# Kernel optimization log

Measured on AMD Instinct MI355X. Metric: run time of the kernel, lower is better.

Reference implementation:

```python
import jax, jax.numpy as jnp
import numpy as np
from jax.scipy.special import gammaln, xlogy

DIM = 1536
HEADS = 8
DK = 64
DV = 64
BS = 128
N = 1536
NRPF = 192  # num_rel_pos_features, divisible by 6
B = 2


def _positional_embed(n, feat):
    # [2n-1, feat] relative positional basis (exponential, central-mask, gamma),
    # each duplicated with sign(d) asymmetric variant.
    f = feat // 6
    d = jnp.arange(-n + 1, n, dtype=jnp.float32)
    ad = jnp.abs(d)[:, None]  # [2n-1, 1]
    # exponential: log-spaced half lives
    half_life = 2.0 ** jnp.linspace(3.0, float(np.log2(n)), f)
    e_exp = jnp.exp(-float(np.log(2.0)) / half_life[None, :] * ad)
    # central mask: 1 if |d| < 2^i - 1
    widths = 2.0 ** jnp.arange(1, f + 1, dtype=jnp.float32) - 1.0
    e_cm = (widths[None, :] > ad).astype(jnp.float32)
    # gamma pdf, linearly spaced means
    std = n / (2.0 * f)
    mean = jnp.linspace(n / f, float(n), f)[None, :]
    conc = (mean / std) ** 2
    rate = mean / (std ** 2)
    log_unnorm = xlogy(conc - 1.0, ad) - rate * ad
    log_norm = gammaln(conc) - conc * jnp.log(rate)
    probs = jnp.exp(log_unnorm - log_norm) + 1e-8
    e_g = probs / jnp.max(probs, axis=-1, keepdims=True)
    emb = jnp.concatenate([e_exp, e_cm, e_g], axis=-1)  # [2n-1, 3f]
    return jnp.concatenate([emb, jnp.sign(d)[:, None] * emb], axis=-1)  # [2n-1, 6f]


def _relative_shift(t):
    # [B, H, N, 2N-1] -> [B, H, N, N] (Transformer-XL shift)
    b, h, t1, t2 = t.shape
    t = jnp.concatenate([jnp.zeros_like(t[..., :1]), t], axis=-1)  # [.., t2+1]
    t = t.reshape(b, h, t2 + 1, t1)[:, :, 1:, :].reshape(b, h, t1, t2)
    return t[..., :t1]


def setup_inputs() -> dict:
    key = jax.random.key(0)
    ks = jax.random.split(key, 10)
    x = jax.random.normal(ks[0], (B, N, DIM), dtype=jnp.float32)
    Wq = jax.random.normal(ks[1], (DIM, HEADS * DK), dtype=jnp.float32) * 0.02
    Wk = jax.random.normal(ks[2], (DIM, HEADS * DK), dtype=jnp.float32) * 0.02
    Wv = jax.random.normal(ks[3], (DIM, HEADS * DV), dtype=jnp.float32) * 0.02
    Wrel = jax.random.normal(ks[4], (NRPF, HEADS * DK), dtype=jnp.float32) * 0.02
    rel_content_bias = jax.random.normal(ks[5], (1, HEADS, 1, DK), dtype=jnp.float32)
    rel_pos_bias = jax.random.normal(ks[6], (1, HEADS, 1, DK), dtype=jnp.float32)
    # to_out is zero-init in the original; use small random so the output/grads are non-trivial
    Wo = jax.random.normal(ks[7], (HEADS * DV, DIM), dtype=jnp.float32) * 0.02
    bo = jnp.zeros((DIM,), dtype=jnp.float32)
    pos_embed = _positional_embed(N, NRPF)  # [2N-1, NRPF]
    # BigBird block-local window mask: blocks bi attend to blocks bi-1..bi+1
    bi = np.arange(N) // BS
    local_mask = jnp.asarray(np.abs(bi[:, None] - bi[None, :]) <= 1)  # [N, N] bool
    # a few global tokens per batch
    is_global = jnp.zeros((B, N), dtype=bool).at[:, :4].set(True)
    return {"x": x, "Wq": Wq, "Wk": Wk, "Wv": Wv, "Wrel": Wrel,
            "rel_content_bias": rel_content_bias, "rel_pos_bias": rel_pos_bias,
            "Wo": Wo, "bo": bo, "pos_embed": pos_embed,
            "local_mask": local_mask, "is_global": is_global}


def reference(x, Wq, Wk, Wv, Wrel, rel_content_bias, rel_pos_bias, Wo, bo,
              pos_embed, local_mask, is_global):
    b, n, _ = x.shape
    h, dk = rel_content_bias.shape[1], rel_content_bias.shape[-1]
    dv = Wv.shape[-1] // h
    scale = dk ** -0.5
    q = (x @ Wq).reshape(b, n, h, dk).transpose(0, 2, 1, 3) * scale  # [b,h,n,dk]
    k = (x @ Wk).reshape(b, n, h, dk).transpose(0, 2, 1, 3)
    v = (x @ Wv).reshape(b, n, h, dv).transpose(0, 2, 1, 3)
    content_logits = jnp.einsum('bhid,bhjd->bhij', q + rel_content_bias, k)
    rel_k = (pos_embed @ Wrel).reshape(2 * n - 1, h, dk).transpose(1, 0, 2)  # [h,2n-1,dk]
    rel_logits = jnp.einsum('bhid,hjd->bhij', q + rel_pos_bias, rel_k)  # [b,h,n,2n-1]
    logits = content_logits + _relative_shift(rel_logits)
    attn_bool = (local_mask[None, None] | is_global[:, None, :, None]
                 | is_global[:, None, None, :])
    logits = jnp.where(attn_bool, logits.astype(jnp.float32), -jnp.inf)
    attn = jax.nn.softmax(logits, axis=-1)
    out = jnp.einsum('bhij,bhjd->bhid', attn, v.astype(jnp.float32))
    out = out.astype(x.dtype).transpose(0, 2, 1, 3).reshape(b, n, h * dv)
    return out @ Wo + bo
```

## Files before the change

### kernel.cpp

```cpp
#include <hip/hip_runtime.h>
#include <math.h>

#define NSEQ 1536
#define HD3  1536
#define RKLD 512
#define RLEN 3071
#define NB   12

typedef __attribute__((ext_vector_type(8))) short bf16x8;
typedef __attribute__((ext_vector_type(4))) float f32x4;
typedef _Float16 f16x8 __attribute__((ext_vector_type(8)));
typedef _Float16 f16x4 __attribute__((ext_vector_type(4)));

__device__ __forceinline__ unsigned short f2bf(float f) {
    union { float f; unsigned u; } v; v.f = f;
    unsigned r = v.u + 0x7fffu + ((v.u >> 16) & 1u);
    return (unsigned short)(r >> 16);
}
__device__ __forceinline__ float bf2f(unsigned short s) {
    union { unsigned u; float f; } v; v.u = ((unsigned)s) << 16;
    return v.f;
}
__device__ __forceinline__ void cp16(const void* g, void* l) {
    __builtin_amdgcn_global_load_lds(
        (const __attribute__((address_space(1))) void*)g,
        (__attribute__((address_space(3))) void*)l, 16, 0, 0);
}

#define KSWZ(row, d) ((row) * 64 + (((((d) >> 3) ^ ((row) & 7))) << 3) + ((d) & 7))
#define PSWZ(r, j)   ((r) * 128 + (((((j) >> 3) ^ ((r) & 15))) << 3) + ((j) & 7))
#define VSTR 136

__global__ __launch_bounds__(256) void splitf16(
    const float* __restrict__ X, _Float16* __restrict__ H, int n4)
{
    int i = blockIdx.x * 256 + threadIdx.x;
    if (i >= n4) return;
    float4 v = ((const float4*)X)[i];
    union { _Float16 h[4]; ushort4 u; } c;
    c.h[0] = (_Float16)v.x; c.h[1] = (_Float16)v.y;
    c.h[2] = (_Float16)v.z; c.h[3] = (_Float16)v.w;
    ((ushort4*)H)[i] = c.u;
}

__device__ __forceinline__ void wsplit_body16(
    const float* __restrict__ W, _Float16* __restrict__ T,
    int K, int N, int n_off, int ldt, float scale, int bx, int by)
{
    __shared__ float tile[64][65];
    const int k0 = by * 64, n0 = bx * 64;
    const int t = threadIdx.x;
    const int rr = t >> 4, c4 = (t & 15) * 4;
#pragma unroll
    for (int p = 0; p < 4; ++p) {
        int r = p * 16 + rr;
        float4 v = *(const float4*)(W + (size_t)(k0 + r) * N + n0 + c4);
        tile[r][c4 + 0] = v.x; tile[r][c4 + 1] = v.y;
        tile[r][c4 + 2] = v.z; tile[r][c4 + 3] = v.w;
    }
    __syncthreads();
#pragma unroll
    for (int p = 0; p < 4; ++p) {
        int n = p * 16 + rr;
        union { _Float16 h[4]; ushort4 u; } cc;
        cc.h[0] = (_Float16)(tile[c4 + 0][n] * scale);
        cc.h[1] = (_Float16)(tile[c4 + 1][n] * scale);
        cc.h[2] = (_Float16)(tile[c4 + 2][n] * scale);
        cc.h[3] = (_Float16)(tile[c4 + 3][n] * scale);
        size_t o = (size_t)(n_off + n0 + n) * ldt + k0 + c4;
        *(ushort4*)(T + o) = cc.u;
    }
}

__global__ __launch_bounds__(256) void wsplit_all(
    const float* __restrict__ Wq, const float* __restrict__ Wk,
    const float* __restrict__ Wv, const float* __restrict__ Wo,
    const float* __restrict__ Wrel,
    _Float16* __restrict__ Tqkv, _Float16* __restrict__ To,
    _Float16* __restrict__ Trel)
{
    const int z = blockIdx.z;
    if (z < 3) {
        const float* W = (z == 0) ? Wq : (z == 1) ? Wk : Wv;
        wsplit_body16(W, Tqkv, 1536, 512, z * 512, 1536,
                      (z == 0) ? 0.125f : 1.f, blockIdx.x, blockIdx.y);
    } else if (z == 3) {
        wsplit_body16(Wo, To, 512, 1536, 0, 512, 1.f, blockIdx.y, blockIdx.x);
    } else {
        if (blockIdx.y >= 3) return;
        wsplit_body16(Wrel, Trel, 192, 512, 0, 192, 1.f, blockIdx.x, blockIdx.y);
    }
}

__global__ __launch_bounds__(256) void gemm_f16k(
    const _Float16* __restrict__ A,
    const _Float16* __restrict__ B,
    const float* __restrict__ bias, float* __restrict__ C,
    int M, int N, int K)
{
    __shared__ _Float16 sA[2][4096];
    __shared__ _Float16 sB[2][4096];
    const int t = threadIdx.x;
    const int wave = t >> 6, lane = t & 63;
    const int nwg = gridDim.x * gridDim.y;
    const int lin = blockIdx.y * gridDim.x + blockIdx.x;
    const int swz = (lin & 7) * (nwg >> 3) + (lin >> 3);
    const int bx = swz % gridDim.x, by = swz / gridDim.x;
    const int m0 = by * 64, n0 = bx * 64;
    const int wm = (wave >> 1) * 32, wn = (wave & 1) * 32;
    const int fr = lane & 15, quad = lane >> 4;

    f32x4 acc[2][2];
#pragma unroll
    for (int i = 0; i < 2; ++i)
#pragma unroll
        for (int j = 0; j < 2; ++j)
#pragma unroll
            for (int c = 0; c < 4; ++c) acc[i][j][c] = 0.f;

    const int nsteps = K >> 6;

#define STAGE(k0, buf)                                                        \
    {                                                                         \
        _Pragma("unroll")                                                     \
        for (int it = 0; it < 2; ++it) {                                      \
            int cidx = it * 256 + t;                                          \
            int row = cidx >> 3, slot = cidx & 7;                             \
            int gch = slot ^ (row & 7);                                       \
            size_t goA = (size_t)(m0 + row) * K + (k0) + gch * 8;             \
            size_t goB = (size_t)(n0 + row) * K + (k0) + gch * 8;             \
            cp16(A + goA, &sA[buf][it * 2048 + wave * 512]);                  \
            cp16(B + goB, &sB[buf][it * 2048 + wave * 512]);                  \
        }                                                                     \
    }

    STAGE(0, 0);
    for (int s = 0; s < nsteps; ++s) {
        const int buf = s & 1;
        __syncthreads();
        if (s + 1 < nsteps) STAGE((s + 1) * 64, buf ^ 1);

        f16x8 fa[2][2], fb[2][2];
#pragma unroll
        for (int ti = 0; ti < 2; ++ti)
#pragma unroll
            for (int kc = 0; kc < 2; ++kc) {
                fa[ti][kc] = *(const f16x8*)&sA[buf][KSWZ(wm + ti * 16 + fr,
                                                          kc * 32 + quad * 8)];
                fb[ti][kc] = *(const f16x8*)&sB[buf][KSWZ(wn + ti * 16 + fr,
                                                          kc * 32 + quad * 8)];
            }
#pragma unroll
        for (int ti = 0; ti < 2; ++ti)
#pragma unroll
            for (int tj = 0; tj < 2; ++tj)
#pragma unroll
                for (int kc = 0; kc < 2; ++kc)
                    acc[ti][tj] = __builtin_amdgcn_mfma_f32_16x16x32_f16(
                        fa[ti][kc], fb[tj][kc], acc[ti][tj], 0, 0, 0);
    }
#undef STAGE

#pragma unroll
    for (int ti = 0; ti < 2; ++ti) {
        int rowb = m0 + wm + ti * 16 + quad * 4;
#pragma unroll
        for (int tj = 0; tj < 2; ++tj) {
            int col = n0 + wn + tj * 16 + fr;
            float bb = bias ? bias[col] : 0.f;
#pragma unroll
            for (int j2 = 0; j2 < 4; ++j2)
                C[(size_t)(rowb + j2) * N + col] = acc[ti][tj][j2] + bb;
        }
    }
}

__global__ __launch_bounds__(256) void drk_kernel(
    const float* __restrict__ rkk, const float* __restrict__ cb,
    const float* __restrict__ rb, float* __restrict__ drk)
{
    int idx = blockIdx.x * 256 + threadIdx.x;
    if (idx >= 8 * RLEN) return;
    int jj = idx >> 3, h = idx & 7;
    const float* rrow = rkk + (size_t)jj * RKLD + h * 64;
    float s0 = 0, s1 = 0, s2 = 0, s3 = 0;
#pragma unroll
    for (int d4 = 0; d4 < 16; ++d4) {
        float4 rv = *(const float4*)(rrow + d4 * 4);
        float dx = rb[h * 64 + d4 * 4 + 0] - cb[h * 64 + d4 * 4 + 0];
        float dy = rb[h * 64 + d4 * 4 + 1] - cb[h * 64 + d4 * 4 + 1];
        float dz = rb[h * 64 + d4 * 4 + 2] - cb[h * 64 + d4 * 4 + 2];
        float dw = rb[h * 64 + d4 * 4 + 3] - cb[h * 64 + d4 * 4 + 3];
        s0 = fmaf(dx, rv.x, s0); s1 = fmaf(dy, rv.y, s1);
        s2 = fmaf(dz, rv.z, s2); s3 = fmaf(dw, rv.w, s3);
    }
    drk[h * RLEN + jj] = (s0 + s1) + (s2 + s3);
}

__global__ __launch_bounds__(256) void relb_mfma(
    const float* __restrict__ qkv, const float* __restrict__ rkk,
    const float* __restrict__ rb, _Float16* __restrict__ relbT)
{
    __shared__ _Float16 sR[8192];
    const int ct = blockIdx.x, bi = blockIdx.y, bh = blockIdx.z;
    const int b = bh >> 3, h = bh & 7;
    const int i0 = bi * 128;
    const int c0 = (bi == 0) ? 0 : (bi - 1) * 128;
    const int jjbase = c0 - i0 - 127 + (NSEQ - 1) + ct * 128;
    const int t = threadIdx.x;
    const int wave = t >> 6, lane = t & 63;
    const int fr = lane & 15, quad = lane >> 4;

#pragma unroll
    for (int it = 0; it < 8; ++it) {
        int lin = it * 256 + t;
        int row = lin >> 4, d4 = (lin & 15) * 4;
        const float* rp = rkk + (size_t)(jjbase + row) * RKLD + h * 64 + d4;
        float4 v = *(const float4*)rp;
        union { _Float16 h[4]; ushort4 u; } cc;
        cc.h[0] = (_Float16)v.x; cc.h[1] = (_Float16)v.y;
        cc.h[2] = (_Float16)v.z; cc.h[3] = (_Float16)v.w;
        *(ushort4*)&sR[KSWZ(row, d4)] = cc.u;
    }
    f16x8 qf[2][2];
    {
        const float* Qg = qkv + ((size_t)(b * NSEQ + i0)) * HD3 + h * 64;
#pragma unroll
        for (int ti = 0; ti < 2; ++ti)
#pragma unroll
            for (int kc = 0; kc < 2; ++kc) {
                int m = wave * 32 + ti * 16 + fr;
                int k8 = kc * 32 + quad * 8;
                const float* qp = Qg + (size_t)m * HD3 + k8;
                const float* cp = rb + h * 64 + k8;
                float4 qa = *(const float4*)qp,  qb = *(const float4*)(qp + 4);
                float4 ca = *(const float4*)cp,  c2 = *(const float4*)(cp + 4);
                _Float16 hx[8] = {
                    (_Float16)(qa.x + ca.x), (_Float16)(qa.y + ca.y),
                    (_Float16)(qa.z + ca.z), (_Float16)(qa.w + ca.w),
                    (_Float16)(qb.x + c2.x), (_Float16)(qb.y + c2.y),
                    (_Float16)(qb.z + c2.z), (_Float16)(qb.w + c2.w)};
                qf[ti][kc] = *(f16x8*)hx;
            }
    }
    __syncthreads();

    f32x4 sacc[2][8];
#pragma unroll
    for (int i = 0; i < 2; ++i)
#pragma unroll
        for (int j = 0; j < 8; ++j)
#pragma unroll
            for (int c = 0; c < 4; ++c) sacc[i][j][c] = 0.f;

#pragma unroll
    for (int kc = 0; kc < 2; ++kc) {
        f16x8 bv[8];
#pragma unroll
        for (int tj = 0; tj < 8; ++tj)
            bv[tj] = *(const f16x8*)&sR[KSWZ(tj * 16 + fr, kc * 32 + quad * 8)];
#pragma unroll
        for (int ti = 0; ti < 2; ++ti)
#pragma unroll
            for (int tj = 0; tj < 8; ++tj)
                sacc[ti][tj] = __builtin_amdgcn_mfma_f32_16x16x32_f16(
                    qf[ti][kc], bv[tj], sacc[ti][tj], 0, 0, 0);
    }

    size_t bb_ = ((size_t)bh * NB + bi) * 512;
#pragma unroll
    for (int ti = 0; ti < 2; ++ti) {
        int mr = wave * 32 + ti * 16 + quad * 4;
#pragma unroll
        for (int tj = 0; tj < 8; ++tj) {
            int ccg = ct * 128 + tj * 16 + fr;
#pragma unroll
            for (int reg = 0; reg < 4; ++reg) {
                int r = mr + reg;
                int jl = ccg - 127 + r;
                if (jl >= 0)
                    relbT[(bb_ + jl) * 128 + r] = (_Float16)sacc[ti][tj][reg];
            }
        }
    }
}

__global__ __launch_bounds__(256) void attn_mfma(
    const float* __restrict__ qkv, const _Float16* __restrict__ relbT,
    const float* __restrict__ rkbuf, const float* __restrict__ drk,
    const float* __restrict__ cb, float* __restrict__ O_part,
    float* __restrict__ l_part)
{
    __shared__ unsigned short sKP[16384];
    __shared__ unsigned short sVt[64 * VSTR];
    __shared__ float p_g[128 * 4];
    __shared__ __align__(16) float vg[4 * 64];
    __shared__ float lg[128];
    const int ct = blockIdx.x, bi = blockIdx.y, bh = blockIdx.z;
    const int b = bh >> 3, h = bh & 7;
    const int i0 = bi * 128;
    const int c0 = (bi == 0) ? 0 : (bi - 1) * 128;
    const int c1 = (bi == NB - 1) ? NSEQ : (bi + 2) * 128;
    const int ctile = c0 + ct * 128;
    const int t = threadIdx.x;
    const int wave = t >> 6, lane = t & 63;
    const int fr = lane & 15, quad = lane >> 4;

    float* Op = O_part + (((size_t)ct * 16 + bh) * NSEQ + i0) * 64;
    float* lp = l_part + ((size_t)ct * 16 + bh) * NSEQ + i0;

    if (ctile >= c1) {
        for (int k2 = t; k2 < 8192; k2 += 256) Op[k2] = 0.f;
        if (t < 128) lp[t] = 0.f;
        return;
    }

    const bool do_g = (ct == 0 && bi >= 2);

    {
        const float* Kg = qkv + ((size_t)(b * NSEQ + ctile)) * HD3 + 512 + h * 64;
#pragma unroll
        for (int it = 0; it < 8; ++it) {
            int lin = it * 256 + t;
            int row = lin >> 4, d4 = (lin & 15) * 4;
            float4 v = *(const float4*)(Kg + (size_t)row * HD3 + d4);
            union { _Float16 h[4]; ushort4 u; } cc;
            cc.h[0] = (_Float16)v.x; cc.h[1] = (_Float16)v.y;
            cc.h[2] = (_Float16)v.z; cc.h[3] = (_Float16)v.w;
            *(ushort4*)&sKP[KSWZ(row, d4)] = cc.u;
        }
    }
    {
        const float* Vg = qkv + ((size_t)(b * NSEQ + ctile)) * HD3 + 1024 + h * 64;
#pragma unroll
        for (int it = 0; it < 2; ++it) {
            int lin = it * 256 + t;
            int r4 = (lin >> 4) * 4, d4 = (lin & 15) * 4;
            float4 v0 = *(const float4*)(Vg + (size_t)(r4 + 0) * HD3 + d4);
            float4 v1 = *(const float4*)(Vg + (size_t)(r4 + 1) * HD3 + d4);
            float4 v2 = *(const float4*)(Vg + (size_t)(r4 + 2) * HD3 + d4);
            float4 v3 = *(const float4*)(Vg + (size_t)(r4 + 3) * HD3 + d4);
            const float* p0 = (const float*)&v0;
            const float* p1 = (const float*)&v1;
            const float* p2 = (const float*)&v2;
            const float* p3 = (const float*)&v3;
#pragma unroll
            for (int dd = 0; dd < 4; ++dd) {
                ushort4 hh;
                hh.x = f2bf(p0[dd]); hh.y = f2bf(p1[dd]);
                hh.z = f2bf(p2[dd]); hh.w = f2bf(p3[dd]);
                *(ushort4*)&sVt[(d4 + dd) * VSTR + r4] = hh;
            }
        }
    }
    if (do_g) {
        if (t < 128) {
            const int r = t;
            const int i = i0 + r;
            const int jjb = NSEQ - 1 - i;
            const float* qrow = qkv + (size_t)(b * NSEQ + i) * HD3 + h * 64;
            const float* krow = qkv + (size_t)(b * NSEQ) * HD3 + 512 + h * 64;
            const float* rrow = rkbuf + (size_t)jjb * RKLD + h * 64;
            float s[4] = {0.f, 0.f, 0.f, 0.f};
#pragma unroll
            for (int d4 = 0; d4 < 16; ++d4) {
                float4 qv = *(const float4*)(qrow + d4 * 4);
                float4 cv = *(const float4*)(cb + h * 64 + d4 * 4);
                float q0 = qv.x + cv.x, q1 = qv.y + cv.y;
                float q2 = qv.z + cv.z, q3 = qv.w + cv.w;
#pragma unroll
                for (int j = 0; j < 4; ++j) {
                    float4 kv = *(const float4*)(krow + (size_t)j * HD3 + d4 * 4);
                    float4 rv = *(const float4*)(rrow + (size_t)j * RKLD + d4 * 4);
                    s[j] = fmaf(q0, kv.x + rv.x, s[j]);
                    s[j] = fmaf(q1, kv.y + rv.y, s[j]);
                    s[j] = fmaf(q2, kv.z + rv.z, s[j]);
                    s[j] = fmaf(q3, kv.w + rv.w, s[j]);
                }
            }
            float l = 0.f;
#pragma unroll
            for (int j = 0; j < 4; ++j) {
                float p = __expf(s[j] + drk[h * RLEN + jjb + j]);
                p_g[r * 4 + j] = p;
                l += p;
            }
            lg[r] = l;
        } else {
            int u = (t - 128) * 2;
#pragma unroll
            for (int w = 0; w < 2; ++w) {
                int idx = u + w;
                vg[idx] = qkv[(size_t)(b * NSEQ + (idx >> 6)) * HD3 + 1024
                              + h * 64 + (idx & 63)];
            }
        }
    }
    f16x8 qf[2][2];
    {
        const float* Qg = qkv + ((size_t)(b * NSEQ + i0)) * HD3 + h * 64;
#pragma unroll
        for (int ti = 0; ti < 2; ++ti)
#pragma unroll
            for (int kc = 0; kc < 2; ++kc) {
                int m = wave * 32 + ti * 16 + fr;
                int k8 = kc * 32 + quad * 8;
                const float* qp = Qg + (size_t)m * HD3 + k8;
                const float* cp = cb + h * 64 + k8;
                float4 qa = *(const float4*)qp,  qb = *(const float4*)(qp + 4);
                float4 ca = *(const float4*)cp,  c2 = *(const float4*)(cp + 4);
                _Float16 hx[8] = {
                    (_Float16)(qa.x + ca.x), (_Float16)(qa.y + ca.y),
                    (_Float16)(qa.z + ca.z), (_Float16)(qa.w + ca.w),
                    (_Float16)(qb.x + c2.x), (_Float16)(qb.y + c2.y),
                    (_Float16)(qb.z + c2.z), (_Float16)(qb.w + c2.w)};
                qf[ti][kc] = *(f16x8*)hx;
            }
    }
    __syncthreads();

    f32x4 sacc[2][8];
#pragma unroll
    for (int i = 0; i < 2; ++i)
#pragma unroll
        for (int j = 0; j < 8; ++j)
#pragma unroll
            for (int c = 0; c < 4; ++c) sacc[i][j][c] = 0.f;

#pragma unroll
    for (int kc = 0; kc < 2; ++kc) {
        f16x8 bv[8];
#pragma unroll
        for (int tj = 0; tj < 8; ++tj)
            bv[tj] = *(const f16x8*)&sKP[KSWZ(tj * 16 + fr, kc * 32 + quad * 8)];
#pragma unroll
        for (int ti = 0; ti < 2; ++ti)
#pragma unroll
            for (int tj = 0; tj < 8; ++tj)
                sacc[ti][tj] = __builtin_amdgcn_mfma_f32_16x16x32_f16(
                    qf[ti][kc], bv[tj], sacc[ti][tj], 0, 0, 0);
    }
    __syncthreads();

    const _Float16* relbase = relbT + (((size_t)bh * NB + bi) * 512 + ct * 128) * 128;
    float lsum[2][4] = {{0.f, 0.f, 0.f, 0.f}, {0.f, 0.f, 0.f, 0.f}};
#pragma unroll
    for (int ti = 0; ti < 2; ++ti) {
        int mr = wave * 32 + ti * 16 + quad * 4;
#pragma unroll
        for (int tj = 0; tj < 8; ++tj) {
            int j = tj * 16 + fr;
            f16x4 rl = *(const f16x4*)&relbase[(size_t)j * 128 + mr];
#pragma unroll
            for (int reg = 0; reg < 4; ++reg) {
                int r = mr + reg;
                float p = __expf(sacc[ti][tj][reg] + (float)rl[reg]);
                unsigned short pb = f2bf(p);
                lsum[ti][reg] += bf2f(pb);
                sKP[PSWZ(r, j)] = pb;
            }
        }
    }
#pragma unroll
    for (int m2 = 1; m2 < 16; m2 <<= 1)
#pragma unroll
        for (int ti = 0; ti < 2; ++ti)
#pragma unroll
            for (int reg = 0; reg < 4; ++reg)
                lsum[ti][reg] += __shfl_xor(lsum[ti][reg], m2, 64);
    if (fr == 0) {
#pragma unroll
        for (int ti = 0; ti < 2; ++ti) {
            int mr = wave * 32 + ti * 16 + quad * 4;
#pragma unroll
            for (int reg = 0; reg < 4; ++reg)
                lp[mr + reg] = lsum[ti][reg] + (do_g ? lg[mr + reg] : 0.f);
        }
    }

    f32x4 oacc[4][2];
#pragma unroll
    for (int i = 0; i < 4; ++i)
#pragma unroll
        for (int j = 0; j < 2; ++j)
#pragma unroll
            for (int c = 0; c < 4; ++c) oacc[i][j][c] = 0.f;

#pragma unroll
    for (int kc = 0; kc < 4; ++kc) {
        bf16x8 pbv[2];
#pragma unroll
        for (int rt2 = 0; rt2 < 2; ++rt2) {
            int r = (wave * 2 + rt2) * 16 + fr;
            pbv[rt2] = *(const bf16x8*)&sKP[PSWZ(r, kc * 32 + quad * 8)];
        }
#pragma unroll
        for (int dt = 0; dt < 4; ++dt) {
            bf16x8 av = *(const bf16x8*)&sVt[(dt * 16 + fr) * VSTR + kc * 32 + quad * 8];
#pragma unroll
            for (int rt2 = 0; rt2 < 2; ++rt2)
                oacc[dt][rt2] = __builtin_amdgcn_mfma_f32_16x16x32_bf16(
                    av, pbv[rt2], oacc[dt][rt2], 0, 0, 0);
        }
    }
#pragma unroll
    for (int rt2 = 0; rt2 < 2; ++rt2) {
        int r = (wave * 2 + rt2) * 16 + fr;
        float pg0 = 0.f, pg1 = 0.f, pg2 = 0.f, pg3 = 0.f;
        if (do_g) {
            pg0 = p_g[r * 4 + 0]; pg1 = p_g[r * 4 + 1];
            pg2 = p_g[r * 4 + 2]; pg3 = p_g[r * 4 + 3];
        }
#pragma unroll
        for (int dt = 0; dt < 4; ++dt) {
            int d = dt * 16 + quad * 4;
            float4 ov = make_float4(oacc[dt][rt2][0], oacc[dt][rt2][1],
                                    oacc[dt][rt2][2], oacc[dt][rt2][3]);
            if (do_g) {
                float4 v0 = *(const float4*)&vg[0 * 64 + d];
                float4 v1 = *(const float4*)&vg[1 * 64 + d];
                float4 v2 = *(const float4*)&vg[2 * 64 + d];
                float4 v3 = *(const float4*)&vg[3 * 64 + d];
                ov.x += pg0 * v0.x + pg1 * v1.x + pg2 * v2.x + pg3 * v3.x;
                ov.y += pg0 * v0.y + pg1 * v1.y + pg2 * v2.y + pg3 * v3.y;
                ov.z += pg0 * v0.z + pg1 * v1.z + pg2 * v2.z + pg3 * v3.z;
                ov.w += pg0 * v0.w + pg1 * v1.w + pg2 * v2.w + pg3 * v3.w;
            }
            *(float4*)(Op + (size_t)r * 64 + d) = ov;
        }
    }
}

__global__ __launch_bounds__(256) void grows_part(
    const float* __restrict__ qkv, const float* __restrict__ rkk,
    const float* __restrict__ drk, const float* __restrict__ cb,
    float* __restrict__ g_O, float* __restrict__ g_l)
{
    __shared__ float qc_s[64];
    __shared__ float p_s[128];
    __shared__ float obuf[4][64];
    __shared__ float lred[2];
    const int chunk = blockIdx.x;
    const int bhi = blockIdx.y;
    const int i = bhi & 3, h = (bhi >> 2) & 7, b = bhi >> 5;
    const int t = threadIdx.x;
    const int c0 = chunk * 128;
    if (t < 64)
        qc_s[t] = qkv[(size_t)(b * NSEQ + i) * HD3 + h * 64 + t] + cb[h * 64 + t];
    __syncthreads();
    if (t < 128) {
        int j = c0 + t;
        const float* krow = qkv + (size_t)(b * NSEQ + j) * HD3 + 512 + h * 64;
        int jj = j - i + (NSEQ - 1);
        const float* rrow = rkk + (size_t)jj * RKLD + h * 64;
        float s0 = 0, s1 = 0, s2 = 0, s3 = 0;
#pragma unroll
        for (int d4 = 0; d4 < 16; ++d4) {
            float4 kv = *(const float4*)(krow + d4 * 4);
            float4 rv = *(const float4*)(rrow + d4 * 4);
            float4 qv = *(const float4*)(&qc_s[d4 * 4]);
            s0 = fmaf(qv.x, kv.x + rv.x, s0);
            s1 = fmaf(qv.y, kv.y + rv.y, s1);
            s2 = fmaf(qv.z, kv.z + rv.z, s2);
            s3 = fmaf(qv.w, kv.w + rv.w, s3);
        }
        float p = __expf((s0 + s1) + (s2 + s3) + drk[h * RLEN + jj]);
        p_s[t] = p;
        float ls = p;
#pragma unroll
        for (int off = 32; off > 0; off >>= 1)
            ls += __shfl_down(ls, off, 64);
        if ((t & 63) == 0) lred[t >> 6] = ls;
    }
    __syncthreads();
    {
        const int d = t & 63, g = t >> 6;
        float a0 = 0, a1 = 0;
        const float* vbase = qkv + (size_t)(b * NSEQ + c0 + g * 32) * HD3 + 1024 + h * 64 + d;
#pragma unroll
        for (int j2 = 0; j2 < 32; j2 += 2) {
            a0 = fmaf(p_s[g * 32 + j2],     vbase[(size_t)j2 * HD3],       a0);
            a1 = fmaf(p_s[g * 32 + j2 + 1], vbase[(size_t)(j2 + 1) * HD3], a1);
        }
        obuf[g][d] = a0 + a1;
    }
    __syncthreads();
    if (t < 64) {
        float o = (obuf[0][t] + obuf[1][t]) + (obuf[2][t] + obuf[3][t]);
        g_O[((size_t)chunk * 64 + bhi) * 64 + t] = o;
        if (t == 0) g_l[chunk * 64 + bhi] = lred[0] + lred[1];
    }
}

__global__ __launch_bounds__(256) void norm_merge(
    const float* __restrict__ O_part, const float* __restrict__ l_part,
    const float* __restrict__ g_O, const float* __restrict__ g_l,
    _Float16* __restrict__ aoh)
{
    const int bh = blockIdx.y, b = bh >> 3, h = bh & 7;
    const int i = blockIdx.x * 16 + (threadIdx.x >> 4);
    const int d4 = threadIdx.x & 15;
    float ox = 0, oy = 0, oz = 0, ow = 0, l = 0;
    if (i < 4) {
        const int bhi = bh * 4 + i;
#pragma unroll
        for (int c = 0; c < 12; ++c) {
            const float* gp = g_O + ((size_t)c * 64 + bhi) * 64 + d4 * 4;
            ox += gp[0]; oy += gp[1]; oz += gp[2]; ow += gp[3];
            l += g_l[c * 64 + bhi];
        }
    } else {
#pragma unroll
        for (int s = 0; s < 3; ++s) {
            const float* Opp = O_part + (((size_t)s * 16 + bh) * NSEQ + i) * 64 + d4 * 4;
            float4 p = *(const float4*)Opp;
            ox += p.x; oy += p.y; oz += p.z; ow += p.w;
            l += l_part[((size_t)s * 16 + bh) * NSEQ + i];
        }
    }
    float inv = 1.f / l;
    union { _Float16 h[4]; ushort4 u; } cc;
    cc.h[0] = (_Float16)(ox * inv); cc.h[1] = (_Float16)(oy * inv);
    cc.h[2] = (_Float16)(oz * inv); cc.h[3] = (_Float16)(ow * inv);
    size_t o = ((size_t)(b * NSEQ + i)) * 512 + h * 64 + d4 * 4;
    *(ushort4*)(aoh + o) = cc.u;
}

extern "C" void kernel_launch(void* const* d_in, const int* in_sizes, int n_in,
                              void* d_out, int out_size, void* d_ws, size_t ws_size,
                              hipStream_t stream)
{
    const float* x    = (const float*)d_in[0];
    const float* Wq   = (const float*)d_in[1];
    const float* Wk   = (const float*)d_in[2];
    const float* Wv   = (const float*)d_in[3];
    const float* Wrel = (const float*)d_in[4];
    const float* cb   = (const float*)d_in[5];
    const float* rb   = (const float*)d_in[6];
    const float* Wo   = (const float*)d_in[7];
    const float* bo   = (const float*)d_in[8];
    const float* pe   = (const float*)d_in[9];
    float* out = (float*)d_out;

    float* ws = (float*)d_ws;
    float* qkv   = ws;
    float* rkbuf = ws + 4718592;
    float* drk   = ws + 6291456;
    _Float16* aoh = (_Float16*)(ws + 6316032);
    _Float16* woh = (_Float16*)(ws + 7888896);
    float* R = ws + 8675328;
    _Float16* relbT = (_Float16*)R;
    _Float16* xh  = (_Float16*)R;
    _Float16* wqh = (_Float16*)(R + 4718592);
    float* g_O = R + 6291456;
    float* g_l = R + 6340608;
    float* O_part = ws + 15753216;
    float* l_part = ws + 20471808;
    _Float16* peh   = (_Float16*)(ws + 20545536);
    _Float16* wrelT = (_Float16*)(ws + 20840448);

    dim3 blk(256);
    splitf16<<<4608, blk, 0, stream>>>(x, xh, 1179648);
    splitf16<<<576, blk, 0, stream>>>(pe, peh, 147408);
    wsplit_all<<<dim3(8, 24, 5), blk, 0, stream>>>(Wq, Wk, Wv, Wo, Wrel,
                                                   wqh, woh, wrelT);
    gemm_f16k<<<dim3(24, 48), blk, 0, stream>>>(xh, wqh, nullptr, qkv,
                                                3072, 1536, 1536);
    gemm_f16k<<<dim3(8, 48), blk, 0, stream>>>(peh, wrelT, nullptr, rkbuf,
                                               3072, 512, 192);
    drk_kernel<<<96, blk, 0, stream>>>(rkbuf, cb, rb, drk);
    relb_mfma<<<dim3(4, 12, 16), blk, 0, stream>>>(qkv, rkbuf, rb, relbT);
    attn_mfma<<<dim3(3, 12, 16), blk, 0, stream>>>(qkv, relbT, rkbuf, drk, cb,
                                                   O_part, l_part);
    grows_part<<<dim3(12, 64), blk, 0, stream>>>(qkv, rkbuf, drk, cb, g_O, g_l);
    norm_merge<<<dim3(96, 16), blk, 0, stream>>>(O_part, l_part, g_O, g_l, aoh);
    gemm_f16k<<<dim3(24, 48), blk, 0, stream>>>(aoh, woh, bo, out,
                                                3072, 1536, 512);
}
```

Baseline: 242.8 us.

## Store QKV and rel-K projections in half precision and load tiles asynchronously

The QKV and relative-key GEMMs now write 16-bit outputs (fp16 for Q/K and rel-K, bf16 for V) instead of fp32. Downstream kernels read these directly, so the per-block fp32-to-half conversions go away and K/rel-K tiles can be copied into LDS with direct global-to-LDS loads. The two input conversion kernels are merged into one launch. This halves intermediate memory traffic at the cost of storing q/k/v and rel-K at reduced precision before the bias add and dot products.

```diff
diff --git a/kernel.cpp b/kernel.cpp
--- a/kernel.cpp
+++ b/kernel.cpp
@@ -21,6 +21,9 @@
     union { unsigned u; float f; } v; v.u = ((unsigned)s) << 16;
     return v.f;
 }
+__device__ __forceinline__ unsigned short f2h(float f) {
+    union { _Float16 h; unsigned short u; } c; c.h = (_Float16)f; return c.u;
+}
 __device__ __forceinline__ void cp16(const void* g, void* l) {
     __builtin_amdgcn_global_load_lds(
         (const __attribute__((address_space(1))) void*)g,
@@ -31,16 +34,25 @@
 #define PSWZ(r, j)   ((r) * 128 + (((((j) >> 3) ^ ((r) & 15))) << 3) + ((j) & 7))
 #define VSTR 136
 
-__global__ __launch_bounds__(256) void splitf16(
-    const float* __restrict__ X, _Float16* __restrict__ H, int n4)
-{
-    int i = blockIdx.x * 256 + threadIdx.x;
-    if (i >= n4) return;
-    float4 v = ((const float4*)X)[i];
+__global__ __launch_bounds__(256) void split2_f16(
+    const float* __restrict__ X, _Float16* __restrict__ HX,
+    const float* __restrict__ P, _Float16* __restrict__ HP)
+{
+    const int bid = blockIdx.x;
+    const float* src; _Float16* dst; int i;
+    if (bid < 4608) {
+        i = bid * 256 + threadIdx.x;
+        src = X; dst = HX;
+    } else {
+        i = (bid - 4608) * 256 + threadIdx.x;
+        if (i >= 147408) return;
+        src = P; dst = HP;
+    }
+    float4 v = ((const float4*)src)[i];
     union { _Float16 h[4]; ushort4 u; } c;
     c.h[0] = (_Float16)v.x; c.h[1] = (_Float16)v.y;
     c.h[2] = (_Float16)v.z; c.h[3] = (_Float16)v.w;
-    ((ushort4*)H)[i] = c.u;
+    ((ushort4*)dst)[i] = c.u;
 }
 
 __device__ __forceinline__ void wsplit_body16(
@@ -95,8 +107,8 @@
 __global__ __launch_bounds__(256) void gemm_f16k(
     const _Float16* __restrict__ A,
     const _Float16* __restrict__ B,
-    const float* __restrict__ bias, float* __restrict__ C,
-    int M, int N, int K)
+    const float* __restrict__ bias, void* __restrict__ C,
+    int M, int N, int K, int omode)
 {
     __shared__ _Float16 sA[2][4096];
     __shared__ _Float16 sB[2][4096];
@@ -161,44 +173,63 @@
     }
 #undef STAGE
 
-#pragma unroll
-    for (int ti = 0; ti < 2; ++ti) {
-        int rowb = m0 + wm + ti * 16 + quad * 4;
-#pragma unroll
-        for (int tj = 0; tj < 2; ++tj) {
-            int col = n0 + wn + tj * 16 + fr;
-            float bb = bias ? bias[col] : 0.f;
-#pragma unroll
-            for (int j2 = 0; j2 < 4; ++j2)
-                C[(size_t)(rowb + j2) * N + col] = acc[ti][tj][j2] + bb;
+    if (omode == 0) {
+        float* Cf = (float*)C;
+#pragma unroll
+        for (int ti = 0; ti < 2; ++ti) {
+            int rowb = m0 + wm + ti * 16 + quad * 4;
+#pragma unroll
+            for (int tj = 0; tj < 2; ++tj) {
+                int col = n0 + wn + tj * 16 + fr;
+                float bb = bias ? bias[col] : 0.f;
+#pragma unroll
+                for (int j2 = 0; j2 < 4; ++j2)
+                    Cf[(size_t)(rowb + j2) * N + col] = acc[ti][tj][j2] + bb;
+            }
+        }
+    } else {
+        unsigned short* Cu = (unsigned short*)C;
+        const bool vb = (omode == 1) && (n0 >= 1024);
+#pragma unroll
+        for (int ti = 0; ti < 2; ++ti) {
+            int rowb = m0 + wm + ti * 16 + quad * 4;
+#pragma unroll
+            for (int tj = 0; tj < 2; ++tj) {
+                int col = n0 + wn + tj * 16 + fr;
+#pragma unroll
+                for (int j2 = 0; j2 < 4; ++j2) {
+                    float v = acc[ti][tj][j2];
+                    Cu[(size_t)(rowb + j2) * N + col] = vb ? f2bf(v) : f2h(v);
+                }
+            }
         }
     }
 }
 
 __global__ __launch_bounds__(256) void drk_kernel(
-    const float* __restrict__ rkk, const float* __restrict__ cb,
+    const _Float16* __restrict__ rkh, const float* __restrict__ cb,
     const float* __restrict__ rb, float* __restrict__ drk)
 {
     int idx = blockIdx.x * 256 + threadIdx.x;
     if (idx >= 8 * RLEN) return;
     int jj = idx >> 3, h = idx & 7;
-    const float* rrow = rkk + (size_t)jj * RKLD + h * 64;
+    const _Float16* rrow = rkh + (size_t)jj * RKLD + h * 64;
     float s0 = 0, s1 = 0, s2 = 0, s3 = 0;
 #pragma unroll
     for (int d4 = 0; d4 < 16; ++d4) {
-        float4 rv = *(const float4*)(rrow + d4 * 4);
+        f16x4 rv = *(const f16x4*)(rrow + d4 * 4);
         float dx = rb[h * 64 + d4 * 4 + 0] - cb[h * 64 + d4 * 4 + 0];
         float dy = rb[h * 64 + d4 * 4 + 1] - cb[h * 64 + d4 * 4 + 1];
         float dz = rb[h * 64 + d4 * 4 + 2] - cb[h * 64 + d4 * 4 + 2];
         float dw = rb[h * 64 + d4 * 4 + 3] - cb[h * 64 + d4 * 4 + 3];
-        s0 = fmaf(dx, rv.x, s0); s1 = fmaf(dy, rv.y, s1);
-        s2 = fmaf(dz, rv.z, s2); s3 = fmaf(dw, rv.w, s3);
+        s0 = fmaf(dx, (float)rv[0], s0); s1 = fmaf(dy, (float)rv[1], s1);
+        s2 = fmaf(dz, (float)rv[2], s2); s3 = fmaf(dw, (float)rv[3], s3);
     }
     drk[h * RLEN + jj] = (s0 + s1) + (s2 + s3);
 }
 
 __global__ __launch_bounds__(256) void relb_mfma(
-    const float* __restrict__ qkv, const float* __restrict__ rkk,
+    const _Float16* __restrict__ qkvh, const _Float16* __restrict__ rkh,
     const float* __restrict__ rb, _Float16* __restrict__ relbT)
 {
     __shared__ _Float16 sR[8192];
@@ -211,35 +242,32 @@
     const int wave = t >> 6, lane = t & 63;
     const int fr = lane & 15, quad = lane >> 4;
 
-#pragma unroll
-    for (int it = 0; it < 8; ++it) {
-        int lin = it * 256 + t;
-        int row = lin >> 4, d4 = (lin & 15) * 4;
-        const float* rp = rkk + (size_t)(jjbase + row) * RKLD + h * 64 + d4;
-        float4 v = *(const float4*)rp;
-        union { _Float16 h[4]; ushort4 u; } cc;
-        cc.h[0] = (_Float16)v.x; cc.h[1] = (_Float16)v.y;
-        cc.h[2] = (_Float16)v.z; cc.h[3] = (_Float16)v.w;
-        *(ushort4*)&sR[KSWZ(row, d4)] = cc.u;
+    {
+        const _Float16* Rg = rkh + (size_t)jjbase * RKLD + h * 64;
+#pragma unroll
+        for (int it = 0; it < 4; ++it) {
+            int cidx = it * 256 + t;
+            int row = cidx >> 3, slot = cidx & 7;
+            int gch = slot ^ (row & 7);
+            cp16(Rg + (size_t)row * RKLD + gch * 8,
+                 &sR[it * 2048 + wave * 512]);
+        }
     }
     f16x8 qf[2][2];
     {
-        const float* Qg = qkv + ((size_t)(b * NSEQ + i0)) * HD3 + h * 64;
+        const _Float16* Qg = qkvh + ((size_t)(b * NSEQ + i0)) * HD3 + h * 64;
 #pragma unroll
         for (int ti = 0; ti < 2; ++ti)
 #pragma unroll
             for (int kc = 0; kc < 2; ++kc) {
                 int m = wave * 32 + ti * 16 + fr;
                 int k8 = kc * 32 + quad * 8;
-                const float* qp = Qg + (size_t)m * HD3 + k8;
+                f16x8 qv = *(const f16x8*)(Qg + (size_t)m * HD3 + k8);
                 const float* cp = rb + h * 64 + k8;
-                float4 qa = *(const float4*)qp,  qb = *(const float4*)(qp + 4);
-                float4 ca = *(const float4*)cp,  c2 = *(const float4*)(cp + 4);
-                _Float16 hx[8] = {
-                    (_Float16)(qa.x + ca.x), (_Float16)(qa.y + ca.y),
-                    (_Float16)(qa.z + ca.z), (_Float16)(qa.w + ca.w),
-                    (_Float16)(qb.x + c2.x), (_Float16)(qb.y + c2.y),
-                    (_Float16)(qb.z + c2.z), (_Float16)(qb.w + c2.w)};
+                _Float16 hx[8];
+#pragma unroll
+                for (int u = 0; u < 8; ++u)
+                    hx[u] = (_Float16)((float)qv[u] + cp[u]);
                 qf[ti][kc] = *(f16x8*)hx;
             }
     }
@@ -286,8 +314,8 @@
 }
 
 __global__ __launch_bounds__(256) void attn_mfma(
-    const float* __restrict__ qkv, const _Float16* __restrict__ relbT,
-    const float* __restrict__ rkbuf, const float* __restrict__ drk,
+    const _Float16* __restrict__ qkvh, const _Float16* __restrict__ relbT,
+    const _Float16* __restrict__ rkh, const float* __restrict__ drk,
     const float* __restrict__ cb, float* __restrict__ O_part,
     float* __restrict__ l_part)
 {
@@ -316,39 +344,38 @@
     }
 
     const bool do_g = (ct == 0 && bi >= 2);
+    const unsigned short* Vall = (const unsigned short*)qkvh;
 
     {
-        const float* Kg = qkv + ((size_t)(b * NSEQ + ctile)) * HD3 + 512 + h * 64;
-#pragma unroll
-        for (int it = 0; it < 8; ++it) {
-            int lin = it * 256 + t;
-            int row = lin >> 4, d4 = (lin & 15) * 4;
-            float4 v = *(const float4*)(Kg + (size_t)row * HD3 + d4);
-            union { _Float16 h[4]; ushort4 u; } cc;
-            cc.h[0] = (_Float16)v.x; cc.h[1] = (_Float16)v.y;
-            cc.h[2] = (_Float16)v.z; cc.h[3] = (_Float16)v.w;
-            *(ushort4*)&sKP[KSWZ(row, d4)] = cc.u;
+        const _Float16* Kg = qkvh + ((size_t)(b * NSEQ + ctile)) * HD3 + 512 + h * 64;
+#pragma unroll
+        for (int it = 0; it < 4; ++it) {
+            int cidx = it * 256 + t;
+            int row = cidx >> 3, slot = cidx & 7;
+            int gch = slot ^ (row & 7);
+            cp16(Kg + (size_t)row * HD3 + gch * 8,
+                 (unsigned short*)&sKP[it * 2048 + wave * 512]);
         }
     }
     {
-        const float* Vg = qkv + ((size_t)(b * NSEQ + ctile)) * HD3 + 1024 + h * 64;
+        const unsigned short* Vg = Vall + ((size_t)(b * NSEQ + ctile)) * HD3
+                                   + 1024 + h * 64;
 #pragma unroll
         for (int it = 0; it < 2; ++it) {
             int lin = it * 256 + t;
             int r4 = (lin >> 4) * 4, d4 = (lin & 15) * 4;
-            float4 v0 = *(const float4*)(Vg + (size_t)(r4 + 0) * HD3 + d4);
-            float4 v1 = *(const float4*)(Vg + (size_t)(r4 + 1) * HD3 + d4);
-            float4 v2 = *(const float4*)(Vg + (size_t)(r4 + 2) * HD3 + d4);
-            float4 v3 = *(const float4*)(Vg + (size_t)(r4 + 3) * HD3 + d4);
-            const float* p0 = (const float*)&v0;
-            const float* p1 = (const float*)&v1;
-            const float* p2 = (const float*)&v2;
-            const float* p3 = (const float*)&v3;
+            ushort4 v0 = *(const ushort4*)(Vg + (size_t)(r4 + 0) * HD3 + d4);
+            ushort4 v1 = *(const ushort4*)(Vg + (size_t)(r4 + 1) * HD3 + d4);
+            ushort4 v2 = *(const ushort4*)(Vg + (size_t)(r4 + 2) * HD3 + d4);
+            ushort4 v3 = *(const ushort4*)(Vg + (size_t)(r4 + 3) * HD3 + d4);
+            const unsigned short* p0 = (const unsigned short*)&v0;
+            const unsigned short* p1 = (const unsigned short*)&v1;
+            const unsigned short* p2 = (const unsigned short*)&v2;
+            const unsigned short* p3 = (const unsigned short*)&v3;
 #pragma unroll
             for (int dd = 0; dd < 4; ++dd) {
                 ushort4 hh;
-                hh.x = f2bf(p0[dd]); hh.y = f2bf(p1[dd]);
-                hh.z = f2bf(p2[dd]); hh.w = f2bf(p3[dd]);
+                hh.x = p0[dd]; hh.y = p1[dd]; hh.z = p2[dd]; hh.w = p3[dd];
                 *(ushort4*)&sVt[(d4 + dd) * VSTR + r4] = hh;
             }
         }
@@ -358,24 +385,24 @@
             const int r = t;
             const int i = i0 + r;
             const int jjb = NSEQ - 1 - i;
-            const float* qrow = qkv + (size_t)(b * NSEQ + i) * HD3 + h * 64;
-            const float* krow = qkv + (size_t)(b * NSEQ) * HD3 + 512 + h * 64;
-            const float* rrow = rkbuf + (size_t)jjb * RKLD + h * 64;
+            const _Float16* qrow = qkvh + (size_t)(b * NSEQ + i) * HD3 + h * 64;
+            const _Float16* krow = qkvh + (size_t)(b * NSEQ) * HD3 + 512 + h * 64;
+            const _Float16* rrow = rkh + (size_t)jjb * RKLD + h * 64;
             float s[4] = {0.f, 0.f, 0.f, 0.f};
 #pragma unroll
             for (int d4 = 0; d4 < 16; ++d4) {
-                float4 qv = *(const float4*)(qrow + d4 * 4);
+                f16x4 qv = *(const f16x4*)(qrow + d4 * 4);
                 float4 cv = *(const float4*)(cb + h * 64 + d4 * 4);
-                float q0 = qv.x + cv.x, q1 = qv.y + cv.y;
-                float q2 = qv.z + cv.z, q3 = qv.w + cv.w;
+                float q0 = (float)qv[0] + cv.x, q1 = (float)qv[1] + cv.y;
+                float q2 = (float)qv[2] + cv.z, q3 = (float)qv[3] + cv.w;
 #pragma unroll
                 for (int j = 0; j < 4; ++j) {
-                    float4 kv = *(const float4*)(krow + (size_t)j * HD3 + d4 * 4);
-                    float4 rv = *(const float4*)(rrow + (size_t)j * RKLD + d4 * 4);
-                    s[j] = fmaf(q0, kv.x + rv.x, s[j]);
-                    s[j] = fmaf(q1, kv.y + rv.y, s[j]);
-                    s[j] = fmaf(q2, kv.z + rv.z, s[j]);
-                    s[j] = fmaf(q3, kv.w + rv.w, s[j]);
+                    f16x4 kv = *(const f16x4*)(krow + (size_t)j * HD3 + d4 * 4);
+                    f16x4 rv = *(const f16x4*)(rrow + (size_t)j * RKLD + d4 * 4);
+                    s[j] = fmaf(q0, (float)kv[0] + (float)rv[0], s[j]);
+                    s[j] = fmaf(q1, (float)kv[1] + (float)rv[1], s[j]);
+                    s[j] = fmaf(q2, (float)kv[2] + (float)rv[2], s[j]);
+                    s[j] = fmaf(q3, (float)kv[3] + (float)rv[3], s[j]);
                 }
             }
             float l = 0.f;
@@ -387,33 +414,31 @@
             }
             lg[r] = l;
         } else {
+            const unsigned short* Vg0 = Vall + (size_t)(b * NSEQ) * HD3
+                                        + 1024 + h * 64;
             int u = (t - 128) * 2;
 #pragma unroll
             for (int w = 0; w < 2; ++w) {
                 int idx = u + w;
-                vg[idx] = qkv[(size_t)(b * NSEQ + (idx >> 6)) * HD3 + 1024
-                              + h * 64 + (idx & 63)];
+                vg[idx] = bf2f(Vg0[(size_t)(idx >> 6) * HD3 + (idx & 63)]);
             }
         }
     }
     f16x8 qf[2][2];
     {
-        const float* Qg = qkv + ((size_t)(b * NSEQ + i0)) * HD3 + h * 64;
+        const _Float16* Qg = qkvh + ((size_t)(b * NSEQ + i0)) * HD3 + h * 64;
 #pragma unroll
         for (int ti = 0; ti < 2; ++ti)
 #pragma unroll
             for (int kc = 0; kc < 2; ++kc) {
                 int m = wave * 32 + ti * 16 + fr;
                 int k8 = kc * 32 + quad * 8;
-                const float* qp = Qg + (size_t)m * HD3 + k8;
+                f16x8 qv = *(const f16x8*)(Qg + (size_t)m * HD3 + k8);
                 const float* cp = cb + h * 64 + k8;
-                float4 qa = *(const float4*)qp,  qb = *(const float4*)(qp + 4);
-                float4 ca = *(const float4*)cp,  c2 = *(const float4*)(cp + 4);
-                _Float16 hx[8] = {
-                    (_Float16)(qa.x + ca.x), (_Float16)(qa.y + ca.y),
-                    (_Float16)(qa.z + ca.z), (_Float16)(qa.w + ca.w),
-                    (_Float16)(qb.x + c2.x), (_Float16)(qb.y + c2.y),
-                    (_Float16)(qb.z + c2.z), (_Float16)(qb.w + c2.w)};
+                _Float16 hx[8];
+#pragma unroll
+                for (int u = 0; u < 8; ++u)
+                    hx[u] = (_Float16)((float)qv[u] + cp[u]);
                 qf[ti][kc] = *(f16x8*)hx;
             }
     }
@@ -532,7 +557,7 @@
 }
 
 __global__ __launch_bounds__(256) void grows_part(
-    const float* __restrict__ qkv, const float* __restrict__ rkk,
+    const _Float16* __restrict__ qkvh, const _Float16* __restrict__ rkh,
     const float* __restrict__ drk, const float* __restrict__ cb,
     float* __restrict__ g_O, float* __restrict__ g_l)
 {
@@ -546,23 +571,24 @@
     const int t = threadIdx.x;
     const int c0 = chunk * 128;
     if (t < 64)
-        qc_s[t] = qkv[(size_t)(b * NSEQ + i) * HD3 + h * 64 + t] + cb[h * 64 + t];
+        qc_s[t] = (float)qkvh[(size_t)(b * NSEQ + i) * HD3 + h * 64 + t]
+                  + cb[h * 64 + t];
     __syncthreads();
     if (t < 128) {
         int j = c0 + t;
-        const float* krow = qkv + (size_t)(b * NSEQ + j) * HD3 + 512 + h * 64;
+        const _Float16* krow = qkvh + (size_t)(b * NSEQ + j) * HD3 + 512 + h * 64;
         int jj = j - i + (NSEQ - 1);
-        const float* rrow = rkk + (size_t)jj * RKLD + h * 64;
+        const _Float16* rrow = rkh + (size_t)jj * RKLD + h * 64;
         float s0 = 0, s1 = 0, s2 = 0, s3 = 0;
 #pragma unroll
         for (int d4 = 0; d4 < 16; ++d4) {
-            float4 kv = *(const float4*)(krow + d4 * 4);
-            float4 rv = *(const float4*)(rrow + d4 * 4);
+            f16x4 kv = *(const f16x4*)(krow + d4 * 4);
+            f16x4 rv = *(const f16x4*)(rrow + d4 * 4);
             float4 qv = *(const float4*)(&qc_s[d4 * 4]);
-            s0 = fmaf(qv.x, kv.x + rv.x, s0);
-            s1 = fmaf(qv.y, kv.y + rv.y, s1);
-            s2 = fmaf(qv.z, kv.z + rv.z, s2);
-            s3 = fmaf(qv.w, kv.w + rv.w, s3);
+            s0 = fmaf(qv.x, (float)kv[0] + (float)rv[0], s0);
+            s1 = fmaf(qv.y, (float)kv[1] + (float)rv[1], s1);
+            s2 = fmaf(qv.z, (float)kv[2] + (float)rv[2], s2);
+            s3 = fmaf(qv.w, (float)kv[3] + (float)rv[3], s3);
         }
         float p = __expf((s0 + s1) + (s2 + s3) + drk[h * RLEN + jj]);
         p_s[t] = p;
@@ -576,11 +602,12 @@
     {
         const int d = t & 63, g = t >> 6;
         float a0 = 0, a1 = 0;
-        const float* vbase = qkv + (size_t)(b * NSEQ + c0 + g * 32) * HD3 + 1024 + h * 64 + d;
+        const unsigned short* vbase = (const unsigned short*)qkvh
+            + (size_t)(b * NSEQ + c0 + g * 32) * HD3 + 1024 + h * 64 + d;
 #pragma unroll
         for (int j2 = 0; j2 < 32; j2 += 2) {
-            a0 = fmaf(p_s[g * 32 + j2],     vbase[(size_t)j2 * HD3],       a0);
-            a1 = fmaf(p_s[g * 32 + j2 + 1], vbase[(size_t)(j2 + 1) * HD3], a1);
+            a0 = fmaf(p_s[g * 32 + j2],     bf2f(vbase[(size_t)j2 * HD3]),       a0);
+            a1 = fmaf(p_s[g * 32 + j2 + 1], bf2f(vbase[(size_t)(j2 + 1) * HD3]), a1);
         }
         obuf[g][d] = a0 + a1;
     }
@@ -643,37 +670,36 @@
     float* out = (float*)d_out;
 
     float* ws = (float*)d_ws;
-    float* qkv   = ws;
-    float* rkbuf = ws + 4718592;
-    float* drk   = ws + 6291456;
-    _Float16* aoh = (_Float16*)(ws + 6316032);
-    _Float16* woh = (_Float16*)(ws + 7888896);
-    float* R = ws + 8675328;
+    _Float16* qkvh = (_Float16*)ws;
+    _Float16* rkh  = (_Float16*)(ws + 2359296);
+    float* drk   = ws + 3145728;
+    _Float16* aoh = (_Float16*)(ws + 3170304);
+    _Float16* woh = (_Float16*)(ws + 3956736);
+    float* R = ws + 4349952;
     _Float16* relbT = (_Float16*)R;
     _Float16* xh  = (_Float16*)R;
-    _Float16* wqh = (_Float16*)(R + 4718592);
+    _Float16* wqh = (_Float16*)(R + 2359296);
     float* g_O = R + 6291456;
     float* g_l = R + 6340608;
-    float* O_part = ws + 15753216;
-    float* l_part = ws + 20471808;
-    _Float16* peh   = (_Float16*)(ws + 20545536);
-    _Float16* wrelT = (_Float16*)(ws + 20840448);
+    float* O_part = ws + 10691328;
+    float* l_part = ws + 15409920;
+    _Float16* peh   = (_Float16*)(ws + 15483648);
+    _Float16* wrelT = (_Float16*)(ws + 15778560);
 
     dim3 blk(256);
-    splitf16<<<4608, blk, 0, stream>>>(x, xh, 1179648);
-    splitf16<<<576, blk, 0, stream>>>(pe, peh, 147408);
+    split2_f16<<<5184, blk, 0, stream>>>(x, xh, pe, peh);
     wsplit_all<<<dim3(8, 24, 5), blk, 0, stream>>>(Wq, Wk, Wv, Wo, Wrel,
                                                    wqh, woh, wrelT);
-    gemm_f16k<<<dim3(24, 48), blk, 0, stream>>>(xh, wqh, nullptr, qkv,
-                                                3072, 1536, 1536);
-    gemm_f16k<<<dim3(8, 48), blk, 0, stream>>>(peh, wrelT, nullptr, rkbuf,
-                                               3072, 512, 192);
-    drk_kernel<<<96, blk, 0, stream>>>(rkbuf, cb, rb, drk);
-    relb_mfma<<<dim3(4, 12, 16), blk, 0, stream>>>(qkv, rkbuf, rb, relbT);
-    attn_mfma<<<dim3(3, 12, 16), blk, 0, stream>>>(qkv, relbT, rkbuf, drk, cb,
+    gemm_f16k<<<dim3(24, 48), blk, 0, stream>>>(xh, wqh, nullptr, qkvh,
+                                                3072, 1536, 1536, 1);
+    gemm_f16k<<<dim3(8, 48), blk, 0, stream>>>(peh, wrelT, nullptr, rkh,
+                                               3072, 512, 192, 2);
+    drk_kernel<<<96, blk, 0, stream>>>(rkh, cb, rb, drk);
+    relb_mfma<<<dim3(4, 12, 16), blk, 0, stream>>>(qkvh, rkh, rb, relbT);
+    attn_mfma<<<dim3(3, 12, 16), blk, 0, stream>>>(qkvh, relbT, rkh, drk, cb,
                                                    O_part, l_part);
-    grows_part<<<dim3(12, 64), blk, 0, stream>>>(qkv, rkbuf, drk, cb, g_O, g_l);
+    grows_part<<<dim3(12, 64), blk, 0, stream>>>(qkvh, rkh, drk, cb, g_O, g_l);
     norm_merge<<<dim3(96, 16), blk, 0, stream>>>(O_part, l_part, g_O, g_l, aoh);
     gemm_f16k<<<dim3(24, 48), blk, 0, stream>>>(aoh, woh, bo, out,
-                                                3072, 1536, 512);
-}
+                                                3072, 1536, 512, 0);
+}
```

Result: faster. 227.3 us (-6.4%).
